# Kernel tuning notes

Measured on AMD Instinct MI355X. Metric: run time of the kernel, lower is better.

The kernel has to match this reference:

```python
import jax, jax.numpy as jnp
import numpy as np

TEMPERATURE = 0.1


def setup_inputs() -> dict:
    key = jax.random.key(0)
    k1, k2 = jax.random.split(key)
    B, D = 4096, 128
    z_i = jax.random.normal(k1, (B, D), dtype=jnp.float32)
    z_j = jax.random.normal(k2, (B, D), dtype=jnp.float32)
    return {"z_i": z_i, "z_j": z_j}


def reference(z_i, z_j):
    B = z_i.shape[0]
    n = 2 * B
    z = jnp.concatenate([z_i, z_j], axis=0)            # [2B, D]
    sim = jnp.matmul(z, z.T) / TEMPERATURE             # [2B, 2B]
    # positives: diag(sim, +B) and diag(sim, -B)
    pos = jnp.concatenate([jnp.diagonal(sim, B), jnp.diagonal(sim, -B)])[:, None]  # [2B, 1]
    # negatives: sim with diagonal removed, row-wise -> [2B, 2B-1]
    # strided trick equivalent to sim[~eye].reshape(n, n-1)
    neg = sim.ravel()[:-1].reshape(n - 1, n + 1)[:, 1:].reshape(n, n - 1)
    logits = jnp.concatenate([pos, neg], axis=1)       # [2B, 2B]
    # cross-entropy with labels all zero (positive in column 0)
    loss = jnp.mean(jax.nn.logsumexp(logits, axis=1) - logits[:, 0])
    return loss
```

## Files before the change

kernel.cpp:

```cpp
#include <hip/hip_runtime.h>
#include <hip/hip_bf16.h>
#include <stdint.h>

#define N_TOT  8192
#define BHALF  4096
#define DDIM   128
#define NSPLIT 16

typedef short bf16x8 __attribute__((ext_vector_type(8)));
typedef float f32x4  __attribute__((ext_vector_type(4)));

__device__ __forceinline__ float ex2(float x) { return __builtin_amdgcn_exp2f(x); }

#define SCALE_C 3.798282440185f

__device__ __forceinline__ ushort2 cvt2(float a, float b) {
    __hip_bfloat162 h = __float22bfloat162_rn(make_float2(a, b));
    return *reinterpret_cast<ushort2*>(&h);
}

__device__ __forceinline__ bf16x8 cvt8(float4 lo, float4 hi) {
    union { bf16x8 v; ushort2 u[4]; } r;
    r.u[0] = cvt2(lo.x * SCALE_C, lo.y * SCALE_C);
    r.u[1] = cvt2(lo.z * SCALE_C, lo.w * SCALE_C);
    r.u[2] = cvt2(hi.x * SCALE_C, hi.y * SCALE_C);
    r.u[3] = cvt2(hi.z * SCALE_C, hi.w * SCALE_C);
    return r.v;
}

__device__ __forceinline__ void gload16(const void* g, void* l) {
    __builtin_amdgcn_global_load_lds(
        (const __attribute__((address_space(1))) void*)g,
        (__attribute__((address_space(3))) void*)l, 16, 0, 0);
}

__launch_bounds__(256)
__global__ void k_prep(const float* __restrict__ zi, const float* __restrict__ zj,
                       unsigned short* __restrict__ zb, float* __restrict__ out) {
    if (blockIdx.x == 0 && threadIdx.x == 0) out[0] = 0.f;
    int gid = blockIdx.x * 256 + threadIdx.x;
    int row = gid >> 4, g = gid & 15;
    const float* rp = (row < BHALF) ? zi + row * DDIM : zj + (row - BHALF) * DDIM;
    float4 lo = *reinterpret_cast<const float4*>(rp + g * 8);
    float4 hi = *reinterpret_cast<const float4*>(rp + g * 8 + 4);
    int slot = g ^ (row & 7);
    *reinterpret_cast<bf16x8*>(&zb[row * DDIM + slot * 8]) = cvt8(lo, hi);
}

__launch_bounds__(512, 4)
__global__ void k_main(const unsigned short* __restrict__ zb,
                       float* __restrict__ pm, float* __restrict__ pl) {
    __shared__ unsigned short lds[2][64 * 128];
    const int tid = threadIdx.x;
    const int w = tid >> 6, lane = tid & 63;
    const int q = lane >> 4, ln = lane & 15;
    const int rb = blockIdx.x >> 4, cs = blockIdx.x & 15;
    const int rowBase = rb * 256 + w * 32;
    const int colBase = cs * 512;

    bf16x8 afr[2][4];
    #pragma unroll
    for (int s = 0; s < 2; ++s) {
        int row = rowBase + s * 16 + ln;
        const unsigned short* rp = zb + row * DDIM;
        int rx = row & 7;
        #pragma unroll
        for (int kc = 0; kc < 4; ++kc)
            afr[s][kc] = *reinterpret_cast<const bf16x8*>(rp + ((kc * 4 + q) ^ rx) * 8);
    }

    float m[2][4], l[2][4];
    #pragma unroll
    for (int s = 0; s < 2; ++s)
        #pragma unroll
        for (int r = 0; r < 4; ++r) { m[s][r] = -1e38f; l[s][r] = 0.f; }

#define STAGE(B, CH) do {                                                     \
        const unsigned short* sp_ = zb + (colBase + (CH) * 64) * DDIM;        \
        gload16(sp_ + (0 * 512 + tid) * 8, &lds[B][0 * 4096 + w * 512]);      \
        gload16(sp_ + (1 * 512 + tid) * 8, &lds[B][1 * 4096 + w * 512]);      \
    } while (0)

    STAGE(0, 0);
    __syncthreads();

    for (int ch = 0; ch < 8; ++ch) {
        const unsigned short* buf = lds[ch & 1];
        if (ch < 7) STAGE((ch + 1) & 1, ch + 1);

        f32x4 acc[2][4];
        #pragma unroll
        for (int s = 0; s < 2; ++s)
            #pragma unroll
            for (int ct = 0; ct < 4; ++ct) acc[s][ct] = (f32x4){0.f, 0.f, 0.f, 0.f};

        #pragma unroll
        for (int ct = 0; ct < 4; ++ct) {
            bf16x8 bfr[4];
            #pragma unroll
            for (int kc = 0; kc < 4; ++kc) {
                int slot = (q + 4 * kc) ^ (ln & 7);
                bfr[kc] = *reinterpret_cast<const bf16x8*>(
                    &buf[(ct * 16 + ln) * 128 + slot * 8]);
            }
            #pragma unroll
            for (int s = 0; s < 2; ++s)
                #pragma unroll
                for (int kc = 0; kc < 4; ++kc)
                    acc[s][ct] = __builtin_amdgcn_mfma_f32_16x16x32_bf16(
                        afr[s][kc], bfr[kc], acc[s][ct], 0, 0, 0);
        }

        const int c0 = colBase + ch * 64;
        #pragma unroll
        for (int s = 0; s < 2; ++s) {
            const int rt = rowBase + s * 16;
            #pragma unroll
            for (int ct = 0; ct < 4; ++ct) {
                if (rt == c0 + ct * 16) {
                    #pragma unroll
                    for (int r = 0; r < 4; ++r)
                        if (ln == q * 4 + r) acc[s][ct][r] = -__builtin_inff();
                }
            }
            #pragma unroll
            for (int r = 0; r < 4; ++r) {
                float t0 = acc[s][0][r], t1 = acc[s][1][r];
                float t2 = acc[s][2][r], t3 = acc[s][3][r];
                float mo = m[s][r];
                float mn = fmaxf(fmaxf(fmaxf(t0, t1), fmaxf(t2, t3)), mo);
                float sc = ex2(mo - mn);
                float pv = (ex2(t0 - mn) + ex2(t1 - mn)) + (ex2(t2 - mn) + ex2(t3 - mn));
                l[s][r] = fmaf(l[s][r], sc, pv);
                m[s][r] = mn;
            }
        }
        __syncthreads();
    }
#undef STAGE

    #pragma unroll
    for (int s = 0; s < 2; ++s) {
        #pragma unroll
        for (int r = 0; r < 4; ++r) {
            float mm = m[s][r], ll = l[s][r];
            #pragma unroll
            for (int msk = 1; msk < 16; msk <<= 1) {
                float om = __shfl_xor(mm, msk, 64);
                float ol = __shfl_xor(ll, msk, 64);
                float mn = fmaxf(mm, om);
                ll = ll * ex2(mm - mn) + ol * ex2(om - mn);
                mm = mn;
            }
            if (ln == 0) {
                int row = rowBase + s * 16 + q * 4 + r;
                pm[cs * N_TOT + row] = mm;
                pl[cs * N_TOT + row] = ll;
            }
        }
    }
}

__global__ void k_finish(const float* __restrict__ zi, const float* __restrict__ zj,
                         const float* __restrict__ pm, const float* __restrict__ pl,
                         float* __restrict__ out) {
    int row = blockIdx.x * 256 + threadIdx.x;
    int pr  = row & (BHALF - 1);
    const float4* a = reinterpret_cast<const float4*>(zi + pr * DDIM);
    const float4* b = reinterpret_cast<const float4*>(zj + pr * DDIM);
    float acc = 0.f;
    #pragma unroll
    for (int k = 0; k < 32; ++k) {
        float4 x = a[k], y = b[k];
        acc += x.x * y.x + x.y * y.y + x.z * y.z + x.w * y.w;
    }
    float p  = 10.f * acc;
    float tp = p * 1.4426950408889634f;
    float mm[NSPLIT];
    float M = tp;
    #pragma unroll
    for (int j = 0; j < NSPLIT; ++j) {
        mm[j] = pm[j * N_TOT + row];
        M = fmaxf(M, mm[j]);
    }
    float S = ex2(tp - M);
    #pragma unroll
    for (int j = 0; j < NSPLIT; ++j)
        S += pl[j * N_TOT + row] * ex2(mm[j] - M);
    float lse = (M + __log2f(S)) * 0.6931471805599453f;
    float li  = lse - p;
    #pragma unroll
    for (int msk = 32; msk; msk >>= 1) li += __shfl_xor(li, msk, 64);
    __shared__ float red[4];
    if ((threadIdx.x & 63) == 0) red[threadIdx.x >> 6] = li;
    __syncthreads();
    if (threadIdx.x == 0)
        atomicAdd(out, (red[0] + red[1] + red[2] + red[3]) * (1.f / 8192.f));
}

extern "C" void kernel_launch(void* const* d_in, const int* in_sizes, int n_in,
                              void* d_out, int out_size, void* d_ws, size_t ws_size,
                              hipStream_t stream) {
    const float* zi = (const float*)d_in[0];
    const float* zj = (const float*)d_in[1];
    float* out = (float*)d_out;
    char* ws = (char*)d_ws;

    unsigned short* zb = (unsigned short*)ws;
    float* pm = (float*)(ws + (size_t)N_TOT * DDIM * 2);
    float* pl = pm + NSPLIT * N_TOT;

    hipLaunchKernelGGL(k_prep,   dim3(512), dim3(256), 0, stream, zi, zj, zb, out);
    hipLaunchKernelGGL(k_main,   dim3(512), dim3(512), 0, stream, zb, pm, pl);
    hipLaunchKernelGGL(k_finish, dim3(32),  dim3(256), 0, stream, zi, zj, pm, pl, out);
}
```

Before: 96.13 us.

## Fuse finish reduction into main kernel via last-block counter; compute positives in prep

Removes the separate k_finish launch. The last of the 16 column-split blocks for each row block now merges the partial max/sum values, computes the per-row loss and atomically adds it to the output. Positive-pair dot products move into k_prep, which already loads z_i, so the finish step no longer re-reads both inputs. This saves one kernel launch and its serial tail, at the cost of an atomic counter, thread fences and extra work in k_prep.

```diff
diff --git a/kernel.cpp b/kernel.cpp
--- a/kernel.cpp
+++ b/kernel.cpp
@@ -6,6 +6,8 @@
 #define BHALF  4096
 #define DDIM   128
 #define NSPLIT 16
+#define LOG2E  1.4426950408889634f
+#define LN2    0.6931471805599453f
 
 typedef short bf16x8 __attribute__((ext_vector_type(8)));
 typedef float f32x4  __attribute__((ext_vector_type(4)));
@@ -36,8 +38,12 @@
 
 __launch_bounds__(256)
 __global__ void k_prep(const float* __restrict__ zi, const float* __restrict__ zj,
-                       unsigned short* __restrict__ zb, float* __restrict__ out) {
-    if (blockIdx.x == 0 && threadIdx.x == 0) out[0] = 0.f;
+                       unsigned short* __restrict__ zb, float* __restrict__ pos,
+                       int* __restrict__ cnt, float* __restrict__ out) {
+    if (blockIdx.x == 0 && threadIdx.x < 32) {
+        cnt[threadIdx.x] = 0;
+        if (threadIdx.x == 0) out[0] = 0.f;
+    }
     int gid = blockIdx.x * 256 + threadIdx.x;
     int row = gid >> 4, g = gid & 15;
     const float* rp = (row < BHALF) ? zi + row * DDIM : zj + (row - BHALF) * DDIM;
@@ -45,11 +51,24 @@
     float4 hi = *reinterpret_cast<const float4*>(rp + g * 8 + 4);
     int slot = g ^ (row & 7);
     *reinterpret_cast<bf16x8*>(&zb[row * DDIM + slot * 8]) = cvt8(lo, hi);
+
+    if (row < BHALF) {
+        const float* qp = zj + row * DDIM + g * 8;
+        float4 ql = *reinterpret_cast<const float4*>(qp);
+        float4 qh = *reinterpret_cast<const float4*>(qp + 4);
+        float d = lo.x * ql.x + lo.y * ql.y + lo.z * ql.z + lo.w * ql.w
+                + hi.x * qh.x + hi.y * qh.y + hi.z * qh.z + hi.w * qh.w;
+        #pragma unroll
+        for (int msk = 1; msk < 16; msk <<= 1) d += __shfl_xor(d, msk, 64);
+        if (g == 0) pos[row] = d;
+    }
 }
 
 __launch_bounds__(512, 4)
 __global__ void k_main(const unsigned short* __restrict__ zb,
-                       float* __restrict__ pm, float* __restrict__ pl) {
+                       float* __restrict__ pm, float* __restrict__ pl,
+                       const float* __restrict__ pos, int* __restrict__ cnt,
+                       float* __restrict__ out) {
     __shared__ unsigned short lds[2][64 * 128];
     const int tid = threadIdx.x;
     const int w = tid >> 6, lane = tid & 63;
@@ -159,43 +178,46 @@
             }
         }
     }
-}
-
-__global__ void k_finish(const float* __restrict__ zi, const float* __restrict__ zj,
-                         const float* __restrict__ pm, const float* __restrict__ pl,
-                         float* __restrict__ out) {
-    int row = blockIdx.x * 256 + threadIdx.x;
-    int pr  = row & (BHALF - 1);
-    const float4* a = reinterpret_cast<const float4*>(zi + pr * DDIM);
-    const float4* b = reinterpret_cast<const float4*>(zj + pr * DDIM);
-    float acc = 0.f;
-    #pragma unroll
-    for (int k = 0; k < 32; ++k) {
-        float4 x = a[k], y = b[k];
-        acc += x.x * y.x + x.y * y.y + x.z * y.z + x.w * y.w;
-    }
-    float p  = 10.f * acc;
-    float tp = p * 1.4426950408889634f;
-    float mm[NSPLIT];
-    float M = tp;
-    #pragma unroll
-    for (int j = 0; j < NSPLIT; ++j) {
-        mm[j] = pm[j * N_TOT + row];
-        M = fmaxf(M, mm[j]);
-    }
-    float S = ex2(tp - M);
-    #pragma unroll
-    for (int j = 0; j < NSPLIT; ++j)
-        S += pl[j * N_TOT + row] * ex2(mm[j] - M);
-    float lse = (M + __log2f(S)) * 0.6931471805599453f;
-    float li  = lse - p;
-    #pragma unroll
-    for (int msk = 32; msk; msk >>= 1) li += __shfl_xor(li, msk, 64);
-    __shared__ float red[4];
-    if ((threadIdx.x & 63) == 0) red[threadIdx.x >> 6] = li;
+
     __syncthreads();
-    if (threadIdx.x == 0)
-        atomicAdd(out, (red[0] + red[1] + red[2] + red[3]) * (1.f / 8192.f));
+    __shared__ int amLast;
+    if (tid == 0) {
+        __threadfence();
+        amLast = (atomicAdd(&cnt[rb], 1) == NSPLIT - 1);
+    }
+    __syncthreads();
+    if (amLast) {
+        __threadfence();
+        float li = 0.f;
+        if (tid < 256) {
+            int row = rb * 256 + tid;
+            float p  = 10.f * pos[row & (BHALF - 1)];
+            float tp = p * LOG2E;
+            float M = tp;
+            float mm[NSPLIT];
+            #pragma unroll
+            for (int j = 0; j < NSPLIT; ++j) {
+                mm[j] = pm[j * N_TOT + row];
+                M = fmaxf(M, mm[j]);
+            }
+            float S = ex2(tp - M);
+            #pragma unroll
+            for (int j = 0; j < NSPLIT; ++j)
+                S += pl[j * N_TOT + row] * ex2(mm[j] - M);
+            li = (M + __log2f(S)) * LN2 - p;
+        }
+        #pragma unroll
+        for (int msk = 32; msk; msk >>= 1) li += __shfl_xor(li, msk, 64);
+        __shared__ float redv[8];
+        if (lane == 0) redv[w] = li;
+        __syncthreads();
+        if (tid == 0) {
+            float t = 0.f;
+            #pragma unroll
+            for (int i = 0; i < 8; ++i) t += redv[i];
+            atomicAdd(out, t * (1.f / 8192.f));
+        }
+    }
 }
 
 extern "C" void kernel_launch(void* const* d_in, const int* in_sizes, int n_in,
@@ -207,10 +229,11 @@
     char* ws = (char*)d_ws;
 
     unsigned short* zb = (unsigned short*)ws;
-    float* pm = (float*)(ws + (size_t)N_TOT * DDIM * 2);
-    float* pl = pm + NSPLIT * N_TOT;
-
-    hipLaunchKernelGGL(k_prep,   dim3(512), dim3(256), 0, stream, zi, zj, zb, out);
-    hipLaunchKernelGGL(k_main,   dim3(512), dim3(512), 0, stream, zb, pm, pl);
-    hipLaunchKernelGGL(k_finish, dim3(32),  dim3(256), 0, stream, zi, zj, pm, pl, out);
-}
+    float* pm  = (float*)(ws + (size_t)N_TOT * DDIM * 2);
+    float* pl  = pm + NSPLIT * N_TOT;
+    float* pos = pl + NSPLIT * N_TOT;
+    int*   cnt = (int*)(pos + BHALF);
+
+    hipLaunchKernelGGL(k_prep, dim3(512), dim3(256), 0, stream, zi, zj, zb, pos, cnt, out);
+    hipLaunchKernelGGL(k_main, dim3(512), dim3(512), 0, stream, zb, pm, pl, pos, cnt, out);
+}
```

Result: slower. 117.8 us (+22.5%).
